# Performance work log

Measured on AMD Instinct MI355X. Metric: run time of the kernel, lower is better.

## Reference

```python
import jax, jax.numpy as jnp
import numpy as np

VOCAB = 400000
DIM = 128        # meta['embed_dim']
NBITS = 2        # bits per code
CODEBOOK = 1 << NBITS   # 4 codebook entries
MASK = CODEBOOK - 1
N_WORDS = VOCAB * DIM * NBITS // 32  # 3,200,000 packed int32 words


def setup_inputs() -> dict:
    key = jax.random.key(0)
    k1, k2, k3 = jax.random.split(key, 3)
    input_ids = jax.random.randint(k1, (64, 4096), 0, VOCAB, dtype=jnp.int64)
    # packed bit array: nonnegative int32 words (top bit clear so >> is logical)
    bit_arr = jax.random.randint(k2, (N_WORDS,), 0, 2147483647, dtype=jnp.int32)
    codebook = jax.random.normal(k3, (CODEBOOK,), dtype=jnp.float32)
    return {"input": input_ids, "bit_arr": bit_arr, "codebook": codebook}


def reference(input, bit_arr, codebook):
    flat = input.reshape(-1).astype(jnp.int32)            # [N]
    # code position for (token, dim): p = token*DIM + dim
    pos = flat[:, None] * DIM + jnp.arange(DIM, dtype=jnp.int32)[None, :]  # [N, DIM]
    bitpos = pos * NBITS
    word = bitpos >> 5            # // 32
    shift = bitpos & 31           # % 32
    codes = (bit_arr[word] >> shift) & MASK               # [N, DIM] in [0, 2^NBITS)
    embeds = codebook[codes]                              # [N, DIM] fp32
    return embeds.reshape(input.shape + (DIM,))
```

## Files before the change

### kernel.cpp

```cpp
#include <hip/hip_runtime.h>
#include <hip/hip_bf16.h>


#define EMB_DIM 128
#define TOK_PER_BLOCK 64
#define BLOCK 256

typedef float vfloat4 __attribute__((ext_vector_type(4)));
typedef int   vint4   __attribute__((ext_vector_type(4)));

__global__ __launch_bounds__(BLOCK) void embed2bit_lds_kernel(
    const int* __restrict__ ids,
    const int* __restrict__ bits,
    const float* __restrict__ cb,
    float* __restrict__ out,
    int n_tokens)
{
    __shared__ int lds_words[TOK_PER_BLOCK * 8];

    const int t0  = blockIdx.x * TOK_PER_BLOCK;
    const int tid = threadIdx.x;

    if (tid < TOK_PER_BLOCK * 2) {
        int t = t0 + (tid >> 1);
        if (t < n_tokens) {
            int tok = ids[t];
            vint4 w = *reinterpret_cast<const vint4*>(
                bits + (long long)tok * 8 + (tid & 1) * 4);
            *reinterpret_cast<vint4*>(&lds_words[tid * 4]) = w;
        }
    }
    __syncthreads();

    const float c0 = cb[0], c1 = cb[1], c2 = cb[2], c3 = cb[3];
    const long long out_base = (long long)t0 * EMB_DIM;
    const int n_items = (n_tokens - t0 >= TOK_PER_BLOCK
                             ? TOK_PER_BLOCK : n_tokens - t0) * 32;

#pragma unroll
    for (int q = 0; q < 8; ++q) {
        int item = q * BLOCK + tid;
        if (item >= n_items) break;
        int word = lds_words[item >> 2];
        int byte = (word >> ((item & 3) * 8)) & 0xff;

        vfloat4 r;
#pragma unroll
        for (int j = 0; j < 4; ++j) {
            int c    = (byte >> (2 * j)) & 3;
            float lo = (c & 1) ? c1 : c0;
            float hi = (c & 1) ? c3 : c2;
            r[j]     = (c & 2) ? hi : lo;
        }
        *reinterpret_cast<vfloat4*>(out + out_base + (long long)item * 4) = r;
    }
}

extern "C" void kernel_launch(void* const* d_in, const int* in_sizes, int n_in,
                              void* d_out, int out_size, void* d_ws, size_t ws_size,
                              hipStream_t stream) {
    const int*   ids  = (const int*)d_in[0];
    const int*   bits = (const int*)d_in[1];
    const float* cb   = (const float*)d_in[2];
    float*       out  = (float*)d_out;

    int n_tokens = in_sizes[0];
    int grid = (n_tokens + TOK_PER_BLOCK - 1) / TOK_PER_BLOCK;

    embed2bit_lds_kernel<<<grid, BLOCK, 0, stream>>>(ids, bits, cb, out, n_tokens);
}
```

Before: 148.7 us.

## Make each wave own its token tile with direct global-to-LDS loads

Restructures the kernel so each wave handles its own 32-token tile. A wave stages its tile's packed words into LDS with the global_load_lds builtin and waits only on its own vmcnt, so the block-wide barrier goes away. The block now covers 128 tokens, so there are half as many blocks, each with more work. The risk is correctness: waiting on vmcnt may not be enough to make direct-to-LDS writes visible to other lanes in the same wave, and the output store is still bound by memory bandwidth.

New measurement: 148.7 us. About the same (-0.0%).

```diff
diff --git a/kernel.cpp b/kernel.cpp
--- a/kernel.cpp
+++ b/kernel.cpp
@@ -1,15 +1,15 @@
 #include <hip/hip_runtime.h>
-#include <hip/hip_bf16.h>
 
 
 #define EMB_DIM 128
-#define TOK_PER_BLOCK 64
+#define TOK_PER_WAVE 32
+#define WAVES_PER_BLOCK 4
+#define TOK_PER_BLOCK (TOK_PER_WAVE * WAVES_PER_BLOCK)
 #define BLOCK 256
 
 typedef float vfloat4 __attribute__((ext_vector_type(4)));
-typedef int   vint4   __attribute__((ext_vector_type(4)));
 
-__global__ __launch_bounds__(BLOCK) void embed2bit_lds_kernel(
+__global__ __launch_bounds__(BLOCK) void embed2bit_wave_kernel(
     const int* __restrict__ ids,
     const int* __restrict__ bits,
     const float* __restrict__ cb,
@@ -18,30 +18,37 @@
 {
     __shared__ int lds_words[TOK_PER_BLOCK * 8];
 
-    const int t0  = blockIdx.x * TOK_PER_BLOCK;
-    const int tid = threadIdx.x;
+    const int tid  = threadIdx.x;
+    const int w    = tid >> 6;
+    const int lane = tid & 63;
 
-    if (tid < TOK_PER_BLOCK * 2) {
-        int t = t0 + (tid >> 1);
-        if (t < n_tokens) {
-            int tok = ids[t];
-            vint4 w = *reinterpret_cast<const vint4*>(
-                bits + (long long)tok * 8 + (tid & 1) * 4);
-            *reinterpret_cast<vint4*>(&lds_words[tid * 4]) = w;
-        }
+    const int tile = blockIdx.x * WAVES_PER_BLOCK + w;
+    const int tb   = tile * TOK_PER_WAVE;
+    if (tb >= n_tokens) return;
+    const int tleft = n_tokens - tb;
+    const int ntok  = tleft < TOK_PER_WAVE ? tleft : TOK_PER_WAVE;
+
+    int* lds_w = lds_words + w * (TOK_PER_WAVE * 8);
+    const int myTok = lane >> 1;
+    if (myTok < ntok) {
+        int tok = ids[tb + myTok];
+        __builtin_amdgcn_global_load_lds(
+            (const __attribute__((address_space(1))) void*)
+                (bits + (long long)tok * 8 + (lane & 1) * 4),
+            (__attribute__((address_space(3))) void*)(lds_w + lane * 4),
+            16, 0, 0);
     }
-    __syncthreads();
+    asm volatile("s_waitcnt vmcnt(0)" ::: "memory");
 
     const float c0 = cb[0], c1 = cb[1], c2 = cb[2], c3 = cb[3];
-    const long long out_base = (long long)t0 * EMB_DIM;
-    const int n_items = (n_tokens - t0 >= TOK_PER_BLOCK
-                             ? TOK_PER_BLOCK : n_tokens - t0) * 32;
+    const long long out_base = (long long)tb * EMB_DIM;
+    const int n_items = ntok * 32;
 
 #pragma unroll
-    for (int q = 0; q < 8; ++q) {
-        int item = q * BLOCK + tid;
+    for (int q = 0; q < 16; ++q) {
+        int item = q * 64 + lane;
         if (item >= n_items) break;
-        int word = lds_words[item >> 2];
+        int word = lds_w[item >> 2];
         int byte = (word >> ((item & 3) * 8)) & 0xff;
 
         vfloat4 r;
@@ -67,5 +74,5 @@
     int n_tokens = in_sizes[0];
     int grid = (n_tokens + TOK_PER_BLOCK - 1) / TOK_PER_BLOCK;
 
-    embed2bit_lds_kernel<<<grid, BLOCK, 0, stream>>>(ids, bits, cb, out, n_tokens);
+    embed2bit_wave_kernel<<<grid, BLOCK, 0, stream>>>(ids, bits, cb, out, n_tokens);
 }
```
